# Kernel optimization log

Measured on AMD Instinct MI355X. Metric: run time of the kernel, lower is better.

Reference implementation:

```python
import jax, jax.numpy as jnp
import numpy as np

# norse LIF/LI defaults, v_th overridden to 0.4 in the module
DT = 0.001
TAU_SYN_INV = 200.0
TAU_MEM_INV = 100.0
V_TH = 0.4
SEQ_LEN = 128
ALPHA = 100.0  # superspike surrogate slope (fwd = heaviside)


def heaviside(x):
    return (x > 0).astype(x.dtype)


def _linear_init(k, out_d, in_d):
    bound = 1.0 / np.sqrt(in_d)
    kw, kb = jax.random.split(k)
    W = jax.random.uniform(kw, (out_d, in_d), jnp.float32, -bound, bound)
    b = jax.random.uniform(kb, (out_d,), jnp.float32, -bound, bound)
    return W, b


def setup_inputs() -> dict:
    key = jax.random.key(0)
    ks = jax.random.split(key, 5)
    B = 4096
    x = jax.random.normal(ks[0], (B, 3, 32, 32), jnp.float32)
    W1, b1 = _linear_init(ks[1], 1536, 3072)
    W2, b2 = _linear_init(ks[2], 256, 1536)
    W3, b3 = _linear_init(ks[3], 10, 256)
    # per-timestep additive noise (0.001 * randn in the original)
    noise = jax.random.normal(ks[4], (SEQ_LEN, B, 10), jnp.float32)
    return dict(x=x, W1=W1, b1=b1, W2=W2, b2=b2, W3=W3, b3=b3, noise=noise)


def reference(x, W1, b1, W2, b2, W3, b3, noise):
    B = x.shape[0]
    xf = x.reshape(B, -1)                      # Flatten
    inp1 = xf @ W1.T + b1                      # constant across timesteps -> hoist

    def lif_step(v, i, inp):
        # norse lif_step: decay v with old i, decay i, spike, reset, then add input current
        v_dec = v + DT * TAU_MEM_INV * (-v + i)
        i_dec = i * (1.0 - DT * TAU_SYN_INV)
        z = heaviside(v_dec - V_TH)
        return z, (1.0 - z) * v_dec, i_dec + inp

    def step(carry, n_t):
        v1, i1, v2, i2, vl, il = carry
        z1, v1, i1 = lif_step(v1, i1, inp1)
        a2 = z1 @ W2.T + b2
        z2, v2, i2 = lif_step(v2, i2, a2)
        a3 = z2 @ W3.T + b3
        # norse li_step: v integrates old i; i decays then receives input
        vl = vl + DT * TAU_MEM_INV * (-vl + il)
        il = il * (1.0 - DT * TAU_SYN_INV) + a3
        return (v1, i1, v2, i2, vl, il), vl + 0.001 * n_t

    init = (
        jnp.zeros((B, 1536), x.dtype), jnp.zeros((B, 1536), x.dtype),
        jnp.zeros((B, 256), x.dtype), jnp.zeros((B, 256), x.dtype),
        jnp.zeros((B, 10), x.dtype), jnp.zeros((B, 10), x.dtype),
    )
    _, voltages = jax.lax.scan(step, init, noise)  # [SEQ_LEN, B, 10]
    return jnp.max(voltages, axis=0)
```

## Files before the change

### kernel.cpp

```cpp
#include <hip/hip_runtime.h>

#define BSZ   4096
#define NIN   3072
#define N1    1536
#define N2    256
#define NO    10
#define SEQ   128

#define DVM  0.1f
#define DIS  0.8f
#define VTH  0.4f

#define W2S1 2.0090963e-04f
#define W2S2 7.9098279e-07f

#define S1X 4.7244094e-02f
#define S2X 1.8600037e-04f
#define S3X 7.3228492e-07f
#define S1W 1.4206453e-04f
#define S2W 5.5931704e-07f
#define S3W 2.2020356e-09f

#define OFF_INP1 0
#define OFF_A3   0
#define OFF_XF   67108864
#define OFF_Z1   67108864
#define OFF_W1F  167772160
#define OFF_Z2   176160768
#define OFF_W2F  196083712

typedef short bf16x8 __attribute__((ext_vector_type(8)));
typedef float f32x4  __attribute__((ext_vector_type(4)));
typedef int   i32x4  __attribute__((ext_vector_type(4)));

__device__ __forceinline__ void gload_lds16(const unsigned short* g, unsigned short* l) {
    __builtin_amdgcn_global_load_lds(
        (const __attribute__((address_space(1))) unsigned int*)g,
        (__attribute__((address_space(3))) unsigned int*)l, 16, 0, 0);
}

__device__ __forceinline__ int q8(float v, float inv) {
    int a = (int)rintf(v * inv);
    return a > 127 ? 127 : (a < -127 ? -127 : a);
}

__global__ __launch_bounds__(256) void prep_x_i8(
        const float* __restrict__ x, signed char* __restrict__ xq) {
    const int idx = blockIdx.x * 256 + threadIdx.x;
    const int lane = idx & 63;
    const int m16 = (idx >> 6) & 255;
    const int ks  = idx >> 14;
    const int row = m16 * 16 + (lane & 15);
    const int k0  = ks * 64 + (lane >> 4) * 16;
    const float* src = x + (size_t)row * NIN + k0;
    union { signed char c[16]; i32x4 v; } q1, q2, q3;
    #pragma unroll
    for (int j = 0; j < 16; j++) {
        float v = src[j];
        v = fminf(fmaxf(v, -6.f), 6.f);
        int a = q8(v, 1.0f / S1X);
        float r1 = fmaf((float)(-a), S1X, v);
        int b = q8(r1, 1.0f / S2X);
        float r2 = fmaf((float)(-b), S2X, r1);
        int c = q8(r2, 1.0f / S3X);
        q1.c[j] = (signed char)a; q2.c[j] = (signed char)b; q3.c[j] = (signed char)c;
    }
    signed char* dst = xq + (size_t)(ks * 256 + m16) * 3072 + lane * 16;
    *(i32x4*)(dst)        = q1.v;
    *(i32x4*)(dst + 1024) = q2.v;
    *(i32x4*)(dst + 2048) = q3.v;
}

__global__ __launch_bounds__(256) void prep_w1_i8(
        const float* __restrict__ W1, signed char* __restrict__ w1q) {
    const int idx = blockIdx.x * 256 + threadIdx.x;
    const int ks  = idx / 6144;
    const int rem = idx % 6144;
    const int n16 = rem >> 6;
    const int lane = rem & 63;
    const int row = n16 * 16 + (lane & 15);
    const int k0  = ks * 64 + (lane >> 4) * 16;
    const float* src = W1 + (size_t)row * NIN + k0;
    union { signed char c[16]; i32x4 v; } q1, q2, q3;
    #pragma unroll
    for (int j = 0; j < 16; j++) {
        float v = src[j];
        int a = q8(v, 1.0f / S1W);
        float r1 = fmaf((float)(-a), S1W, v);
        int b = q8(r1, 1.0f / S2W);
        float r2 = fmaf((float)(-b), S2W, r1);
        int c = q8(r2, 1.0f / S3W);
        q1.c[j] = (signed char)a; q2.c[j] = (signed char)b; q3.c[j] = (signed char)c;
    }
    signed char* dst = w1q + ((size_t)ks * 12 + (n16 >> 3)) * 24576
                           + (n16 & 7) * 3072 + lane * 16;
    *(i32x4*)(dst)        = q1.v;
    *(i32x4*)(dst + 1024) = q2.v;
    *(i32x4*)(dst + 2048) = q3.v;
}

__global__ __launch_bounds__(256, 3) void gemm1_i8(
        const signed char* __restrict__ xq, const signed char* __restrict__ w1q,
        const float* __restrict__ b1, float* __restrict__ inp1) {
    __shared__ signed char Bs[2][24576];
    const int tx = threadIdx.x;
    const int wave = tx >> 6, lane = tx & 63;
    const int wm = wave >> 1, wn = wave & 1;
    const int ln = lane & 15, ko = lane >> 4;
    const int bid = blockIdx.x;
    const int wg = (bid & 7) * 96 + (bid >> 3);
    const int mtile = wg / 12, ntile = wg % 12;
    const int m16b = mtile * 4 + wm * 2;

    i32x4 acc[2][4][3];
    #pragma unroll
    for (int mt = 0; mt < 2; mt++)
        #pragma unroll
        for (int nt = 0; nt < 4; nt++)
            #pragma unroll
            for (int d = 0; d < 3; d++) acc[mt][nt][d] = (i32x4){0,0,0,0};

    const signed char* xbase = xq + lane * 16;

#define ALOADI(A_, ks_) do {                                                  \
    _Pragma("unroll")                                                         \
    for (int mt_ = 0; mt_ < 2; mt_++)                                         \
        _Pragma("unroll")                                                     \
        for (int d_ = 0; d_ < 3; d_++)                                        \
            A_[mt_][d_] = *(const i32x4*)(xbase +                             \
                (size_t)((ks_) * 256 + m16b + mt_) * 3072 + d_ * 1024);       \
} while (0)

#define STAGEI(ks_, buf_) do {                                                \
    const signed char* s_ = w1q + ((size_t)(ks_) * 12 + ntile) * 24576        \
                                + wave * 6144 + lane * 16;                    \
    signed char* d_ = &Bs[buf_][wave * 6144];                                 \
    _Pragma("unroll")                                                         \
    for (int j_ = 0; j_ < 6; j_++)                                            \
        gload_lds16((const unsigned short*)(s_ + j_ * 1024),                  \
                    (unsigned short*)(d_ + j_ * 1024));                       \
} while (0)

#define COMPI(A_, buf_) do {                                                  \
    _Pragma("unroll")                                                         \
    for (int nt_ = 0; nt_ < 4; nt_++) {                                       \
        const signed char* bp_ = &Bs[buf_][(wn * 4 + nt_) * 3072 + lane * 16];\
        i32x4 e1 = *(const i32x4*)(bp_);                                      \
        i32x4 e2 = *(const i32x4*)(bp_ + 1024);                               \
        i32x4 e3 = *(const i32x4*)(bp_ + 2048);                               \
        _Pragma("unroll")                                                     \
        for (int mt_ = 0; mt_ < 2; mt_++) {                                   \
            acc[mt_][nt_][0] = __builtin_amdgcn_mfma_i32_16x16x64_i8(A_[mt_][0], e1, acc[mt_][nt_][0], 0, 0, 0); \
            acc[mt_][nt_][1] = __builtin_amdgcn_mfma_i32_16x16x64_i8(A_[mt_][0], e2, acc[mt_][nt_][1], 0, 0, 0); \
            acc[mt_][nt_][1] = __builtin_amdgcn_mfma_i32_16x16x64_i8(A_[mt_][1], e1, acc[mt_][nt_][1], 0, 0, 0); \
            acc[mt_][nt_][2] = __builtin_amdgcn_mfma_i32_16x16x64_i8(A_[mt_][0], e3, acc[mt_][nt_][2], 0, 0, 0); \
            acc[mt_][nt_][2] = __builtin_amdgcn_mfma_i32_16x16x64_i8(A_[mt_][1], e2, acc[mt_][nt_][2], 0, 0, 0); \
            acc[mt_][nt_][2] = __builtin_amdgcn_mfma_i32_16x16x64_i8(A_[mt_][2], e1, acc[mt_][nt_][2], 0, 0, 0); \
        }                                                                     \
    }                                                                         \
} while (0)

    i32x4 aA[2][3];
    STAGEI(0, 0);
    __syncthreads();

    for (int ks = 0; ks < 48; ks++) {
        const int buf = ks & 1;
        ALOADI(aA, ks);
        if (ks + 1 < 48) STAGEI(ks + 1, buf ^ 1);
        COMPI(aA, buf);
        __syncthreads();
    }

    const float S11 = S1X * S1W;
    #pragma unroll
    for (int nt = 0; nt < 4; nt++) {
        const int n = ntile * 128 + wn * 64 + nt * 16 + ln;
        const float bias = b1[n];
        #pragma unroll
        for (int mt = 0; mt < 2; mt++) {
            #pragma unroll
            for (int r = 0; r < 4; r++) {
                const int m = mtile * 64 + wm * 32 + mt * 16 + ko * 4 + r;
                float f = (float)acc[mt][nt][0][r]
                        + (1.0f / 254.0f)   * (float)acc[mt][nt][1][r]
                        + (1.0f / 64516.0f) * (float)acc[mt][nt][2][r];
                inp1[(size_t)m * N1 + n] = fmaf(f, S11, bias);
            }
        }
    }
#undef ALOADI
#undef STAGEI
#undef COMPI
}

__global__ __launch_bounds__(256) void lif1_kernel(
        const float* __restrict__ inp1, unsigned long long* __restrict__ z1d) {
    const int b = blockIdx.y;
    const int n = blockIdx.x * 256 + threadIdx.x;
    const int lane = threadIdx.x & 63;
    const int w = n >> 6;
    const float inp = inp1[(size_t)b * N1 + n];
    float v = 0.f, i = 0.f;
    unsigned int u[4];
    #pragma unroll
    for (int s = 0; s < 4; s++) {
        unsigned int acc = 0;
        #pragma unroll
        for (int k = 0; k < 32; k++) {
            float vd = v + DVM * (i - v);
            bool z = (vd - VTH) > 0.f;
            acc = (acc << 1) | (z ? 1u : 0u);
            v = z ? 0.f : vd;
            i = DIS * i + inp;
        }
        u[s] = acc;
    }
    unsigned long long X0 = ((unsigned long long)u[0] << 32) | u[1];
    unsigned long long X1 = ((unsigned long long)u[2] << 32) | u[3];
    #pragma unroll
    for (int s = 0; s < 6; s++) {
        const int j = 32 >> s;
        const unsigned long long m =
            (s == 0) ? 0x00000000FFFFFFFFull :
            (s == 1) ? 0x0000FFFF0000FFFFull :
            (s == 2) ? 0x00FF00FF00FF00FFull :
            (s == 3) ? 0x0F0F0F0F0F0F0F0Full :
            (s == 4) ? 0x3333333333333333ull : 0x5555555555555555ull;
        unsigned long long p0 = __shfl_xor(X0, j, 64);
        unsigned long long p1 = __shfl_xor(X1, j, 64);
        if (lane & j) {
            X0 = (X0 & m) | ((p0 << j) & ~m);
            X1 = (X1 & m) | ((p1 << j) & ~m);
        } else {
            X0 = (X0 & ~m) | ((p0 >> j) & m);
            X1 = (X1 & ~m) | ((p1 >> j) & m);
        }
    }
    unsigned long long Y0 = ((unsigned long long)__builtin_bitreverse32((unsigned int)X0) << 32)
                          | __builtin_bitreverse32((unsigned int)(X0 >> 32));
    unsigned long long Y1 = ((unsigned long long)__builtin_bitreverse32((unsigned int)X1) << 32)
                          | __builtin_bitreverse32((unsigned int)(X1 >> 32));
    const int bg = b >> 7, bl = b & 127;
    unsigned long long* zb = z1d + ((size_t)(bg * 24 + w) * 128) * 128 + bl;
    zb[(size_t)lane * 128]        = Y0;
    zb[(size_t)(64 + lane) * 128] = Y1;
}

__global__ __launch_bounds__(256) void prep_w2_i8(
        const float* __restrict__ W2, signed char* __restrict__ frag) {
    const int idx = blockIdx.x * 256 + threadIdx.x;
    const int lane = idx & 63;
    const int nt8  = (idx >> 6) & 7;
    const int chunk = idx >> 9;
    const int nblk = chunk & 1, w = chunk >> 1;
    const int n = (nblk * 8 + nt8) * 16 + (lane & 15);
    const int k0 = w * 64 + (lane >> 4) * 16;
    const float* src = W2 + (size_t)n * N1 + k0;
    union { signed char c[16]; i32x4 v; } q1, q2;
    #pragma unroll
    for (int j = 0; j < 16; j++) {
        float x = src[j];
        int a = (int)rintf(x * (1.0f / W2S1));
        a = a > 127 ? 127 : (a < -127 ? -127 : a);
        float r = x - (float)a * W2S1;
        int b = (int)rintf(r * (1.0f / W2S2));
        b = b > 127 ? 127 : (b < -127 ? -127 : b);
        q1.c[j] = (signed char)a;
        q2.c[j] = (signed char)b;
    }
    signed char* dst = frag + (size_t)chunk * 16384 + nt8 * 2048 + lane * 16;
    *(i32x4*)(dst)        = q1.v;
    *(i32x4*)(dst + 1024) = q2.v;
}

__global__ __launch_bounds__(256, 1) void fused_l2(
        const unsigned long long* __restrict__ z1d,
        const signed char* __restrict__ w2q,
        const float* __restrict__ b2,
        unsigned int* __restrict__ z2h) {
    __shared__ signed char Bs[98304];
    const int tx = threadIdx.x;
    const int wave = tx >> 6, lane = tx & 63;
    const int ko = lane >> 4, ln = lane & 15;
    const int btile = blockIdx.x & 63;
    const int otile = blockIdx.x >> 6;
    const int o0 = otile * 32;

    {
        const int nblk = otile >> 2, nt8_0 = (otile & 3) * 2;
        const signed char* s0 = w2q + (size_t)nblk * 16384 + nt8_0 * 2048 + tx * 16;
        #pragma unroll 4
        for (int w = 0; w < 24; w++)
            gload_lds16((const unsigned short*)(s0 + (size_t)w * 32768),
                        (unsigned short*)(Bs + w * 4096 + tx * 16));
    }
    __syncthreads();

    float v2[2][4] = {{0.f,0.f,0.f,0.f},{0.f,0.f,0.f,0.f}};
    float i2[2][4] = {{0.f,0.f,0.f,0.f},{0.f,0.f,0.f,0.f}};
    float bb2[2];
    bb2[0] = b2[o0 + ln];
    bb2[1] = b2[o0 + 16 + ln];

    const int bg = btile >> 1;
    const size_t zb0 = (size_t)(bg * 24) * 16384 + (btile & 1) * 64 + wave * 16 + ln;
    const size_t zoutb = (size_t)btile * 64 + wave * 16;

    i32x4 acc[2][2];
    #pragma unroll
    for (int nt = 0; nt < 2; nt++)
        #pragma unroll
        for (int d = 0; d < 2; d++) acc[nt][d] = (i32x4){0,0,0,0};

#define LOADZH(Z_, t_, wlo_) do {                                             \
    _Pragma("unroll")                                                         \
    for (int w_ = 0; w_ < 12; w_++)                                           \
        Z_[w_] = z1d[zb0 + (size_t)((wlo_) + w_) * 16384 + (size_t)(t_) * 128]; \
} while (0)

#define COMPH(Z_, wbase_) do {                                                \
    _Pragma("unroll")                                                         \
    for (int w_ = 0; w_ < 12; w_++) {                                         \
        unsigned int bits_ = (unsigned int)(Z_[w_] >> (ko * 16)) & 0xFFFFu;   \
        i32x4 af_;                                                            \
        _Pragma("unroll")                                                     \
        for (int j4_ = 0; j4_ < 4; j4_++)                                     \
            af_[j4_] = (int)((((bits_ >> (j4_ * 4)) & 0xFu) * 0x00204081u) & 0x01010101u); \
        _Pragma("unroll")                                                     \
        for (int nt_ = 0; nt_ < 2; nt_++) {                                   \
            const signed char* bp_ = Bs + ((wbase_) + w_) * 4096 + nt_ * 2048 + lane * 16; \
            i32x4 e1_ = *(const i32x4*)(bp_);                                 \
            i32x4 e2_ = *(const i32x4*)(bp_ + 1024);                          \
            acc[nt_][0] = __builtin_amdgcn_mfma_i32_16x16x64_i8(af_, e1_, acc[nt_][0], 0, 0, 0); \
            acc[nt_][1] = __builtin_amdgcn_mfma_i32_16x16x64_i8(af_, e2_, acc[nt_][1], 0, 0, 0); \
        }                                                                     \
    }                                                                         \
} while (0)

    unsigned long long zwA[12], zwB[12];
    LOADZH(zwA, 0, 0);

    for (int t = 0; t < SEQ; t++) {
        LOADZH(zwB, t, 12);
        COMPH(zwA, 0);
        if (t + 1 < SEQ) LOADZH(zwA, t + 1, 0);
        COMPH(zwB, 12);

        bool zz[2][4];
        #pragma unroll
        for (int nt = 0; nt < 2; nt++) {
            #pragma unroll
            for (int r = 0; r < 4; r++) {
                float a2v = fmaf((float)acc[nt][0][r], W2S1,
                            fmaf((float)acc[nt][1][r], W2S2, bb2[nt]));
                float vd = v2[nt][r] + DVM * (i2[nt][r] - v2[nt][r]);
                bool z = (vd - VTH) > 0.f;
                zz[nt][r] = z;
                v2[nt][r] = z ? 0.f : vd;
                i2[nt][r] = DIS * i2[nt][r] + a2v;
            }
            acc[nt][0] = (i32x4){0,0,0,0};
            acc[nt][1] = (i32x4){0,0,0,0};
        }
        unsigned int* zout = z2h + (size_t)(t * 8 + otile) * BSZ + zoutb;
        #pragma unroll
        for (int r = 0; r < 4; r++) {
            unsigned long long m0 = __ballot(zz[0][r]);
            unsigned long long m1 = __ballot(zz[1][r]);
            unsigned int word = (unsigned int)((m0 >> (ko * 16)) & 0xFFFFull)
                              | ((unsigned int)((m1 >> (ko * 16)) & 0xFFFFull) << 16);
            if (ln == r) zout[ko * 4 + r] = word;
        }
    }
#undef LOADZH
#undef COMPH
}

__global__ __launch_bounds__(256) void gemm3_kernel(
        const unsigned int* __restrict__ z2h, const float* __restrict__ W3,
        const float* __restrict__ b3, float* __restrict__ a3) {
    const int idx = blockIdx.x * 256 + threadIdx.x;
    const int t = idx >> 12, b = idx & 4095;
    unsigned int zw[8];
    #pragma unroll
    for (int g = 0; g < 8; g++) zw[g] = z2h[(size_t)(t * 8 + g) * BSZ + b];
    float acc[NO];
    #pragma unroll
    for (int o = 0; o < NO; o++) acc[o] = b3[o];
    #pragma unroll
    for (int g = 0; g < 8; g++) {
        unsigned int wg = zw[g];
        for (int kb = 0; kb < 32; kb++) {
            float bit = (float)((wg >> kb) & 1u);
            #pragma unroll
            for (int o = 0; o < NO; o++)
                acc[o] = fmaf(bit, W3[o * N2 + g * 32 + kb], acc[o]);
        }
    }
    #pragma unroll
    for (int o = 0; o < NO; o++) a3[(size_t)idx * NO + o] = acc[o];
}

__global__ __launch_bounds__(256) void li_kernel(
        const float* __restrict__ a3, const float* __restrict__ noise,
        float* __restrict__ out) {
    const int idx = blockIdx.x * 256 + threadIdx.x;
    if (idx >= BSZ * NO) return;
    float vl = 0.f, il = 0.f, mx = -1e30f;
    for (int t = 0; t < SEQ; t++) {
        float a = a3[(size_t)t * (BSZ * NO) + idx];
        float vn = vl + DVM * (il - vl);
        il = DIS * il + a;
        vl = vn;
        mx = fmaxf(mx, vl + 0.001f * noise[(size_t)t * (BSZ * NO) + idx]);
    }
    out[idx] = mx;
}

extern "C" void kernel_launch(void* const* d_in, const int* in_sizes, int n_in,
                              void* d_out, int out_size, void* d_ws, size_t ws_size,
                              hipStream_t stream) {
    const float* x     = (const float*)d_in[0];
    const float* W1    = (const float*)d_in[1];
    const float* b1    = (const float*)d_in[2];
    const float* W2    = (const float*)d_in[3];
    const float* b2    = (const float*)d_in[4];
    const float* W3    = (const float*)d_in[5];
    const float* b3    = (const float*)d_in[6];
    const float* noise = (const float*)d_in[7];
    float* out = (float*)d_out;

    char* ws = (char*)d_ws;
    float* inp1 = (float*)(ws + OFF_INP1);
    float* a3   = (float*)(ws + OFF_A3);
    signed char* xq  = (signed char*)(ws + OFF_XF);
    signed char* w1q = (signed char*)(ws + OFF_W1F);
    unsigned long long* z1 = (unsigned long long*)(ws + OFF_Z1);
    unsigned int* z2h = (unsigned int*)(ws + OFF_Z2);
    signed char* w2q = (signed char*)(ws + OFF_W2F);

    dim3 blk(256);
    prep_x_i8<<<dim3(3072), blk, 0, stream>>>(x, xq);
    prep_w1_i8<<<dim3(1152), blk, 0, stream>>>(W1, w1q);
    prep_w2_i8<<<dim3(96), blk, 0, stream>>>(W2, w2q);
    gemm1_i8<<<dim3(768), blk, 0, stream>>>(xq, w1q, b1, inp1);
    lif1_kernel<<<dim3(N1/256, BSZ), blk, 0, stream>>>(inp1, z1);
    fused_l2<<<dim3(512), blk, 0, stream>>>(z1, w2q, b2, z2h);
    gemm3_kernel<<<dim3(SEQ * BSZ / 256), blk, 0, stream>>>(z2h, W3, b3, a3);
    li_kernel<<<dim3((BSZ * NO + 255) / 256), blk, 0, stream>>>(a3, noise, out);
}
```

Before: 1.022 ms.

## Double fused_l2 block size to 512 threads and swizzle block-to-tile mapping

The fused layer-2 kernel now runs 256 blocks of 512 threads (eight waves, each covering 16 batch rows, so a block spans 128 batch rows) instead of 512 blocks of 256 threads. The block index is swizzled so neighbouring blocks share a batch tile across output tiles. The W2 shared-memory preload is redistributed over the larger block. The nibble-to-byte spike expansion is also rewritten with shifts and masks instead of a multiply. The intent is to reuse spike loads across more waves and improve cache locality, at the cost of fewer independent blocks and a launch-bounds change that may constrain registers.

```diff
diff --git a/kernel.cpp b/kernel.cpp
--- a/kernel.cpp
+++ b/kernel.cpp
@@ -274,7 +274,7 @@
     *(i32x4*)(dst + 1024) = q2.v;
 }
 
-__global__ __launch_bounds__(256, 1) void fused_l2(
+__global__ __launch_bounds__(512, 2) void fused_l2(
         const unsigned long long* __restrict__ z1d,
         const signed char* __restrict__ w2q,
         const float* __restrict__ b2,
@@ -283,17 +283,23 @@
     const int tx = threadIdx.x;
     const int wave = tx >> 6, lane = tx & 63;
     const int ko = lane >> 4, ln = lane & 15;
-    const int btile = blockIdx.x & 63;
-    const int otile = blockIdx.x >> 6;
+    const int bid = blockIdx.x;
+    const int work = (bid & 7) * 32 + (bid >> 3);
+    const int btile = work >> 3;
+    const int otile = work & 7;
     const int o0 = otile * 32;
 
     {
         const int nblk = otile >> 2, nt8_0 = (otile & 3) * 2;
-        const signed char* s0 = w2q + (size_t)nblk * 16384 + nt8_0 * 2048 + tx * 16;
-        #pragma unroll 4
-        for (int w = 0; w < 24; w++)
-            gload_lds16((const unsigned short*)(s0 + (size_t)w * 32768),
-                        (unsigned short*)(Bs + w * 4096 + tx * 16));
+        #pragma unroll
+        for (int i = 0; i < 12; i++) {
+            const int idx = i * 512 + tx;
+            const int w = idx >> 8;
+            const int off = (idx & 255) * 16;
+            const signed char* s_ = w2q + (size_t)(w * 2 + nblk) * 16384
+                                        + nt8_0 * 2048 + off;
+            gload_lds16((const unsigned short*)s_, (unsigned short*)(Bs + w * 4096 + off));
+        }
     }
     __syncthreads();
 
@@ -303,9 +309,8 @@
     bb2[0] = b2[o0 + ln];
     bb2[1] = b2[o0 + 16 + ln];
 
-    const int bg = btile >> 1;
-    const size_t zb0 = (size_t)(bg * 24) * 16384 + (btile & 1) * 64 + wave * 16 + ln;
-    const size_t zoutb = (size_t)btile * 64 + wave * 16;
+    const size_t zb0 = (size_t)btile * 24 * 16384 + wave * 16 + ln;
+    const size_t zoutb = (size_t)btile * 128 + wave * 16;
 
     i32x4 acc[2][2];
     #pragma unroll
@@ -325,8 +330,11 @@
         unsigned int bits_ = (unsigned int)(Z_[w_] >> (ko * 16)) & 0xFFFFu;   \
         i32x4 af_;                                                            \
         _Pragma("unroll")                                                     \
-        for (int j4_ = 0; j4_ < 4; j4_++)                                     \
-            af_[j4_] = (int)((((bits_ >> (j4_ * 4)) & 0xFu) * 0x00204081u) & 0x01010101u); \
+        for (int j4_ = 0; j4_ < 4; j4_++) {                                   \
+            unsigned int nib_ = (bits_ >> (j4_ * 4)) & 0xFu;                  \
+            unsigned int x_ = (nib_ | (nib_ << 14)) & 0x00030003u;            \
+            af_[j4_] = (int)((x_ | (x_ << 7)) & 0x01010101u);                 \
+        }                                                                     \
         _Pragma("unroll")                                                     \
         for (int nt_ = 0; nt_ < 2; nt_++) {                                   \
             const signed char* bp_ = Bs + ((wbase_) + w_) * 4096 + nt_ * 2048 + lane * 16; \
@@ -446,7 +454,7 @@
     prep_w2_i8<<<dim3(96), blk, 0, stream>>>(W2, w2q);
     gemm1_i8<<<dim3(768), blk, 0, stream>>>(xq, w1q, b1, inp1);
     lif1_kernel<<<dim3(N1/256, BSZ), blk, 0, stream>>>(inp1, z1);
-    fused_l2<<<dim3(512), blk, 0, stream>>>(z1, w2q, b2, z2h);
+    fused_l2<<<dim3(256), dim3(512), 0, stream>>>(z1, w2q, b2, z2h);
     gemm3_kernel<<<dim3(SEQ * BSZ / 256), blk, 0, stream>>>(z2h, W3, b3, a3);
     li_kernel<<<dim3((BSZ * NO + 255) / 256), blk, 0, stream>>>(a3, noise, out);
 }
```

After: 2.967 ms. 190% more time.

## Halve fused_l2 output tile to double block count and occupancy

Applied to the files above, without the earlier changes.

Each fused_l2 block now covers 16 layer-2 neurons instead of 32. That halves its shared-memory weight slice to 48KB and allows two blocks per CU, with twice as many blocks in the grid. The spike bit-packing moves from 32-bit to 16-bit words, and gemm3 is adapted to read 16 half-words per sample. The nibble-to-byte expansion also swaps a multiply for shift/or operations. The cost is that each block reloads the z1 spike stream for half as much output work, which doubles z1 global traffic.

```diff
diff --git a/kernel.cpp b/kernel.cpp
--- a/kernel.cpp
+++ b/kernel.cpp
@@ -274,44 +274,44 @@
     *(i32x4*)(dst + 1024) = q2.v;
 }
 
-__global__ __launch_bounds__(256, 1) void fused_l2(
+__global__ __launch_bounds__(256, 2) void fused_l2(
         const unsigned long long* __restrict__ z1d,
         const signed char* __restrict__ w2q,
         const float* __restrict__ b2,
-        unsigned int* __restrict__ z2h) {
-    __shared__ signed char Bs[98304];
+        unsigned short* __restrict__ z2hh) {
+    __shared__ signed char Bs[49152];
     const int tx = threadIdx.x;
     const int wave = tx >> 6, lane = tx & 63;
     const int ko = lane >> 4, ln = lane & 15;
     const int btile = blockIdx.x & 63;
     const int otile = blockIdx.x >> 6;
-    const int o0 = otile * 32;
+    const int o0 = otile * 16;
 
     {
-        const int nblk = otile >> 2, nt8_0 = (otile & 3) * 2;
-        const signed char* s0 = w2q + (size_t)nblk * 16384 + nt8_0 * 2048 + tx * 16;
-        #pragma unroll 4
-        for (int w = 0; w < 24; w++)
-            gload_lds16((const unsigned short*)(s0 + (size_t)w * 32768),
-                        (unsigned short*)(Bs + w * 4096 + tx * 16));
+        const int nblk = otile >> 3, nt8 = otile & 7;
+        #pragma unroll
+        for (int i = 0; i < 12; i++) {
+            const int idx = i * 256 + tx;
+            const int w = idx >> 7;
+            const int off = (idx & 127) * 16;
+            const signed char* s_ = w2q + (size_t)(w * 2 + nblk) * 16384
+                                        + nt8 * 2048 + off;
+            gload_lds16((const unsigned short*)s_, (unsigned short*)(Bs + w * 2048 + off));
+        }
     }
     __syncthreads();
 
-    float v2[2][4] = {{0.f,0.f,0.f,0.f},{0.f,0.f,0.f,0.f}};
-    float i2[2][4] = {{0.f,0.f,0.f,0.f},{0.f,0.f,0.f,0.f}};
-    float bb2[2];
-    bb2[0] = b2[o0 + ln];
-    bb2[1] = b2[o0 + 16 + ln];
+    float v2[4] = {0.f, 0.f, 0.f, 0.f};
+    float i2[4] = {0.f, 0.f, 0.f, 0.f};
+    const float bb2 = b2[o0 + ln];
 
     const int bg = btile >> 1;
     const size_t zb0 = (size_t)(bg * 24) * 16384 + (btile & 1) * 64 + wave * 16 + ln;
     const size_t zoutb = (size_t)btile * 64 + wave * 16;
 
-    i32x4 acc[2][2];
-    #pragma unroll
-    for (int nt = 0; nt < 2; nt++)
-        #pragma unroll
-        for (int d = 0; d < 2; d++) acc[nt][d] = (i32x4){0,0,0,0};
+    i32x4 acc[2];
+    acc[0] = (i32x4){0,0,0,0};
+    acc[1] = (i32x4){0,0,0,0};
 
 #define LOADZH(Z_, t_, wlo_) do {                                             \
     _Pragma("unroll")                                                         \
@@ -325,16 +325,16 @@
         unsigned int bits_ = (unsigned int)(Z_[w_] >> (ko * 16)) & 0xFFFFu;   \
         i32x4 af_;                                                            \
         _Pragma("unroll")                                                     \
-        for (int j4_ = 0; j4_ < 4; j4_++)                                     \
-            af_[j4_] = (int)((((bits_ >> (j4_ * 4)) & 0xFu) * 0x00204081u) & 0x01010101u); \
-        _Pragma("unroll")                                                     \
-        for (int nt_ = 0; nt_ < 2; nt_++) {                                   \
-            const signed char* bp_ = Bs + ((wbase_) + w_) * 4096 + nt_ * 2048 + lane * 16; \
-            i32x4 e1_ = *(const i32x4*)(bp_);                                 \
-            i32x4 e2_ = *(const i32x4*)(bp_ + 1024);                          \
-            acc[nt_][0] = __builtin_amdgcn_mfma_i32_16x16x64_i8(af_, e1_, acc[nt_][0], 0, 0, 0); \
-            acc[nt_][1] = __builtin_amdgcn_mfma_i32_16x16x64_i8(af_, e2_, acc[nt_][1], 0, 0, 0); \
+        for (int j4_ = 0; j4_ < 4; j4_++) {                                   \
+            unsigned int nib_ = (bits_ >> (j4_ * 4)) & 0xFu;                  \
+            unsigned int x_ = (nib_ | (nib_ << 14)) & 0x00030003u;            \
+            af_[j4_] = (int)((x_ | (x_ << 7)) & 0x01010101u);                 \
         }                                                                     \
+        const signed char* bp_ = Bs + ((wbase_) + w_) * 2048 + lane * 16;     \
+        i32x4 e1_ = *(const i32x4*)(bp_);                                     \
+        i32x4 e2_ = *(const i32x4*)(bp_ + 1024);                              \
+        acc[0] = __builtin_amdgcn_mfma_i32_16x16x64_i8(af_, e1_, acc[0], 0, 0, 0); \
+        acc[1] = __builtin_amdgcn_mfma_i32_16x16x64_i8(af_, e2_, acc[1], 0, 0, 0); \
     }                                                                         \
 } while (0)
 
@@ -347,29 +347,25 @@
         if (t + 1 < SEQ) LOADZH(zwA, t + 1, 0);
         COMPH(zwB, 12);
 
-        bool zz[2][4];
-        #pragma unroll
-        for (int nt = 0; nt < 2; nt++) {
-            #pragma unroll
-            for (int r = 0; r < 4; r++) {
-                float a2v = fmaf((float)acc[nt][0][r], W2S1,
-                            fmaf((float)acc[nt][1][r], W2S2, bb2[nt]));
-                float vd = v2[nt][r] + DVM * (i2[nt][r] - v2[nt][r]);
-                bool z = (vd - VTH) > 0.f;
-                zz[nt][r] = z;
-                v2[nt][r] = z ? 0.f : vd;
-                i2[nt][r] = DIS * i2[nt][r] + a2v;
-            }
-            acc[nt][0] = (i32x4){0,0,0,0};
-            acc[nt][1] = (i32x4){0,0,0,0};
-        }
-        unsigned int* zout = z2h + (size_t)(t * 8 + otile) * BSZ + zoutb;
+        bool zz[4];
         #pragma unroll
         for (int r = 0; r < 4; r++) {
-            unsigned long long m0 = __ballot(zz[0][r]);
-            unsigned long long m1 = __ballot(zz[1][r]);
-            unsigned int word = (unsigned int)((m0 >> (ko * 16)) & 0xFFFFull)
-                              | ((unsigned int)((m1 >> (ko * 16)) & 0xFFFFull) << 16);
+            float a2v = fmaf((float)acc[0][r], W2S1,
+                        fmaf((float)acc[1][r], W2S2, bb2));
+            float vd = v2[r] + DVM * (i2[r] - v2[r]);
+            bool z = (vd - VTH) > 0.f;
+            zz[r] = z;
+            v2[r] = z ? 0.f : vd;
+            i2[r] = DIS * i2[r] + a2v;
+        }
+        acc[0] = (i32x4){0,0,0,0};
+        acc[1] = (i32x4){0,0,0,0};
+
+        unsigned short* zout = z2hh + (size_t)(t * 16 + otile) * BSZ + zoutb;
+        #pragma unroll
+        for (int r = 0; r < 4; r++) {
+            unsigned long long m0 = __ballot(zz[r]);
+            unsigned short word = (unsigned short)((m0 >> (ko * 16)) & 0xFFFFull);
             if (ln == r) zout[ko * 4 + r] = word;
         }
     }
@@ -378,24 +374,24 @@
 }
 
 __global__ __launch_bounds__(256) void gemm3_kernel(
-        const unsigned int* __restrict__ z2h, const float* __restrict__ W3,
+        const unsigned short* __restrict__ z2hh, const float* __restrict__ W3,
         const float* __restrict__ b3, float* __restrict__ a3) {
     const int idx = blockIdx.x * 256 + threadIdx.x;
     const int t = idx >> 12, b = idx & 4095;
-    unsigned int zw[8];
-    #pragma unroll
-    for (int g = 0; g < 8; g++) zw[g] = z2h[(size_t)(t * 8 + g) * BSZ + b];
+    unsigned short zw[16];
+    #pragma unroll
+    for (int g = 0; g < 16; g++) zw[g] = z2hh[(size_t)(t * 16 + g) * BSZ + b];
     float acc[NO];
     #pragma unroll
     for (int o = 0; o < NO; o++) acc[o] = b3[o];
     #pragma unroll
-    for (int g = 0; g < 8; g++) {
+    for (int g = 0; g < 16; g++) {
         unsigned int wg = zw[g];
-        for (int kb = 0; kb < 32; kb++) {
+        for (int kb = 0; kb < 16; kb++) {
             float bit = (float)((wg >> kb) & 1u);
             #pragma unroll
             for (int o = 0; o < NO; o++)
-                acc[o] = fmaf(bit, W3[o * N2 + g * 32 + kb], acc[o]);
+                acc[o] = fmaf(bit, W3[o * N2 + g * 16 + kb], acc[o]);
         }
     }
     #pragma unroll
@@ -437,7 +433,7 @@
     signed char* xq  = (signed char*)(ws + OFF_XF);
     signed char* w1q = (signed char*)(ws + OFF_W1F);
     unsigned long long* z1 = (unsigned long long*)(ws + OFF_Z1);
-    unsigned int* z2h = (unsigned int*)(ws + OFF_Z2);
+    unsigned short* z2hh = (unsigned short*)(ws + OFF_Z2);
     signed char* w2q = (signed char*)(ws + OFF_W2F);
 
     dim3 blk(256);
@@ -446,7 +442,7 @@
     prep_w2_i8<<<dim3(96), blk, 0, stream>>>(W2, w2q);
     gemm1_i8<<<dim3(768), blk, 0, stream>>>(xq, w1q, b1, inp1);
     lif1_kernel<<<dim3(N1/256, BSZ), blk, 0, stream>>>(inp1, z1);
-    fused_l2<<<dim3(512), blk, 0, stream>>>(z1, w2q, b2, z2h);
-    gemm3_kernel<<<dim3(SEQ * BSZ / 256), blk, 0, stream>>>(z2h, W3, b3, a3);
+    fused_l2<<<dim3(1024), blk, 0, stream>>>(z1, w2q, b2, z2hh);
+    gemm3_kernel<<<dim3(SEQ * BSZ / 256), blk, 0, stream>>>(z2hh, W3, b3, a3);
     li_kernel<<<dim3((BSZ * NO + 255) / 256), blk, 0, stream>>>(a3, noise, out);
 }
```

After: 1.373 ms. 1.34x slower.
